# Optimization experiments

Hardware: AMD Instinct MI355X
Metric: run time of the kernel (lower is better)

Reference implementation:

```python
import jax, jax.numpy as jnp
import numpy as np

S = 2048   # seq_len
E = 1024   # embed_dim
N = 16     # num_heads
H = 64     # head_dim
CL = 1024  # context_length (sliding window)
BASE = 10000.0


def _rope(x, positions, base=BASE):
    # x: (seq, heads, head_dim); even/odd interleaved rotation per RotaryEmbedding
    hd = x.shape[-1]
    dim = hd // 2
    freqs = jnp.exp(-jnp.arange(dim, dtype=x.dtype) * (np.log(base) / dim))
    angles = positions.astype(x.dtype)[:, None] * freqs[None, :]  # (seq, dim)
    cos = jnp.cos(angles)[:, None, :]
    sin = jnp.sin(angles)[:, None, :]
    xe = x[..., ::2]
    xo = x[..., 1::2]
    re = xe * cos - xo * sin
    ro = xe * sin + xo * cos
    return jnp.zeros_like(x).at[..., ::2].set(re).at[..., 1::2].set(ro)


def setup_inputs() -> dict:
    key = jax.random.key(0)
    ks = jax.random.split(key, 9)
    scale = 1.0 / np.sqrt(E)  # keep logits O(1) like eqx.nn.Linear init
    x = jax.random.normal(ks[0], (S, E), jnp.float32)
    Wq = jax.random.normal(ks[1], (E, E), jnp.float32) * scale
    Wk = jax.random.normal(ks[2], (E, E), jnp.float32) * scale
    Wv = jax.random.normal(ks[3], (E, E), jnp.float32) * scale
    Wo = jax.random.normal(ks[4], (E, E), jnp.float32) * scale
    bq = jax.random.normal(ks[5], (E,), jnp.float32) * 0.01
    bk = jax.random.normal(ks[6], (E,), jnp.float32) * 0.01
    bv = jax.random.normal(ks[7], (E,), jnp.float32) * 0.01
    bo = jax.random.normal(ks[8], (E,), jnp.float32) * 0.01
    k_cache = jnp.zeros((CL - 1, N, H), jnp.float32)
    v_cache = jnp.zeros((CL - 1, N, H), jnp.float32)
    return {"x": x, "Wq": Wq, "bq": bq, "Wk": Wk, "bk": bk, "Wv": Wv,
            "bv": bv, "Wo": Wo, "bo": bo, "k_cache": k_cache,
            "v_cache": v_cache, "position": 0}


def reference(x, Wq, bq, Wk, bk, Wv, bv, Wo, bo, k_cache, v_cache, position):
    seq, emb = x.shape
    clm1, n, h = k_cache.shape  # context_length - 1
    cl = clm1 + 1
    # QKV projections (eqx.nn.Linear: W @ x + b, weight is (out, in))
    q = (x @ Wq.T + bq).reshape(seq, n, h)
    k = (x @ Wk.T + bk).reshape(seq, n, h)
    v = (x @ Wv.T + bv).reshape(seq, n, h)
    # RoPE offset by cache position
    pos = jnp.arange(seq) + position
    q = _rope(q, pos)
    k = _rope(k, pos)
    # Append to cache
    k = jnp.concatenate([k_cache, k], axis=0)  # (seq + cl - 1, n, h)
    v = jnp.concatenate([v_cache, v], axis=0)
    # Sliding-window + causal mask, exactly as SelfAttentionBlock.init_mask
    in_dim = seq + clm1
    m = jnp.tril(jnp.ones((in_dim, seq)))
    neg = 1.0 - jnp.tril(jnp.ones((in_dim, seq)), -cl)
    mask = (m * neg).astype(bool).T  # (seq_q, kv_len)
    # Masked SDPA (same math as jax.nn.dot_product_attention with bool mask)
    scores = jnp.einsum('qnh,knh->nqk', q, k) / jnp.sqrt(jnp.asarray(h, q.dtype))
    scores = jnp.where(mask[None], scores, jnp.asarray(-1e30, scores.dtype))
    attn = jax.nn.softmax(scores, axis=-1)
    o = jnp.einsum('nqk,knh->qnh', attn, v).reshape(seq, n * h)
    out = o @ Wo.T + bo
    new_k = k[-(cl - 1):]
    new_v = v[-(cl - 1):]
    return (out, new_k, new_v)
```

## Files before the change

kernel.cpp:

```cpp
#include <hip/hip_runtime.h>
#include <hip/hip_bf16.h>
#include <stdint.h>

#define SQ   2048
#define EMB  1024
#define NH   16
#define HD   64
#define CLM1 1023
#define KTOT 3071
#define KR   3136

typedef __attribute__((ext_vector_type(8))) short short8;
typedef __attribute__((ext_vector_type(4))) float f32x4;

__device__ __forceinline__ short bf16s(float f) {
  __hip_bfloat16 h = __float2bfloat16(f);
  return *reinterpret_cast<short*>(&h);
}

__device__ __forceinline__ float fexp2(float x) {
  float r;
  asm("v_exp_f32 %0, %1" : "=v"(r) : "v"(x));
  return r;
}

#define GLOAD16(g, l) __builtin_amdgcn_global_load_lds( \
    (const __attribute__((address_space(1))) void*)(g), \
    (__attribute__((address_space(3))) void*)(l), 16, 0, 0)

__global__ __launch_bounds__(256) void k_prep(const float* __restrict__ x,
                                              const float* __restrict__ Wq,
                                              const float* __restrict__ Wk,
                                              const float* __restrict__ Wv,
                                              const float* __restrict__ Wo,
                                              const float* __restrict__ bq,
                                              const float* __restrict__ bk,
                                              const float* __restrict__ bv,
                                              const float* __restrict__ kc,
                                              short* __restrict__ xb,
                                              short* __restrict__ wqkvb,
                                              short* __restrict__ wob,
                                              float* __restrict__ bqkv,
                                              short* __restrict__ Kc) {
  const int b = blockIdx.x;
  const int tid = threadIdx.x;
  if (b < 2048) {
    int i = b * 256 + tid;
    float4 v = ((const float4*)x)[i];
    short4 o; o.x = bf16s(v.x); o.y = bf16s(v.y); o.z = bf16s(v.z); o.w = bf16s(v.w);
    ((short4*)xb)[i] = o;
  } else if (b < 5120) {
    int i = (b - 2048) * 256 + tid;
    int seg = i >> 18;
    int loc = i & 262143;
    const float* W = (seg == 0) ? Wq : (seg == 1) ? Wk : Wv;
    float4 v = ((const float4*)W)[loc];
    short4 o; o.x = bf16s(v.x); o.y = bf16s(v.y); o.z = bf16s(v.z); o.w = bf16s(v.w);
    ((short4*)wqkvb)[i] = o;
  } else if (b < 6144) {
    int i = (b - 5120) * 256 + tid;
    float4 v = ((const float4*)Wo)[i];
    short4 o; o.x = bf16s(v.x); o.y = bf16s(v.y); o.z = bf16s(v.z); o.w = bf16s(v.w);
    ((short4*)wob)[i] = o;
  } else if (b < 10236) {
    int idx = (b - 6144) * 256 + tid;
    int h = idx & 63;
    int n = (idx >> 6) & 15;
    int i = idx >> 10;
    Kc[((size_t)n * KR + i) * HD + h] = bf16s(kc[idx]);
  } else {
    int i = (b - 10236) * 256 + tid;
    if (i < 3 * EMB) {
      float v = (i < EMB) ? bq[i] : (i < 2 * EMB) ? bk[i - EMB] : bv[i - 2 * EMB];
      bqkv[i] = v;
    }
  }
}

__global__ __launch_bounds__(256) void k_vt(const float* __restrict__ vc,
                                            const float* __restrict__ qkv,
                                            short* __restrict__ Vt,
                                            float* __restrict__ nv) {
  const int n = blockIdx.y;
  const int i0 = blockIdx.x * 64;
  const int tid = threadIdx.x;
  __shared__ short T[64][66];
  const int h = tid & 63;
  const int iq = tid >> 6;
#pragma unroll
  for (int e = 0; e < 16; ++e) {
    int il = iq + 4 * e;
    int i = i0 + il;
    float v;
    if (i < CLM1)      v = vc[((size_t)i * NH + n) * HD + h];
    else if (i < KTOT) v = qkv[(size_t)(i - CLM1) * (3 * EMB) + 2 * EMB + n * HD + h];
    else               v = 0.0f;
    T[il][h] = bf16s(v);
    if (i >= 2048 && i < KTOT)
      nv[((size_t)(i - 2048) * NH + n) * HD + h] = v;
  }
  __syncthreads();
  const int h2 = tid >> 2;
  const int c0 = (tid & 3) * 16;
  short* dst = &Vt[((size_t)n * HD + h2) * KR + i0 + c0];
#pragma unroll
  for (int c = 0; c < 2; ++c) {
    short8 o;
#pragma unroll
    for (int e = 0; e < 8; ++e) o[e] = T[c0 + c * 8 + e][h2];
    *(short8*)&dst[c * 8] = o;
  }
}

__global__ __launch_bounds__(256) void k_gemm(const short* __restrict__ A,
                                              const short* __restrict__ B,
                                              const float* __restrict__ bias,
                                              float* __restrict__ C,
                                              int M, int N, int K) {
  __shared__ short As[4][128 * 32];
  __shared__ short Bs[4][128 * 32];
  const int tid = threadIdx.x;
  const int lane = tid & 63;
  const int wid = tid >> 6;
  const int wr = wid >> 1, wc = wid & 1;
  const int row0 = blockIdx.x * 128, col0 = blockIdx.y * 128;
  const int lr = lane & 15;
  const int lk = (lane >> 4) * 8;
  const int sr = tid >> 2;
  const int sc = (tid & 3) * 8;
  const short* Ag = A + (size_t)(row0 + sr) * K + sc;
  const short* Bg = B + (size_t)(col0 + sr) * K + sc;

  f32x4 acc[4][4] = {};

#define GSTAGE(k0_, b_) { \
    GLOAD16(Ag + (k0_),                  &As[b_][tid * 8]); \
    GLOAD16(Ag + (size_t)64 * K + (k0_), &As[b_][2048 + tid * 8]); \
    GLOAD16(Bg + (k0_),                  &Bs[b_][tid * 8]); \
    GLOAD16(Bg + (size_t)64 * K + (k0_), &Bs[b_][2048 + tid * 8]); }

  const int nk = K >> 5;
  GSTAGE(0, 0);
  GSTAGE(32, 1);
  for (int ki = 0; ki < nk; ++ki) {
    int kp = (ki + 2 < nk) ? ki + 2 : nk - 1;
    GSTAGE(kp * 32, (ki + 2) & 3);
    asm volatile("s_waitcnt vmcnt(8)" ::: "memory");
    __builtin_amdgcn_s_barrier();
    const short* Ab = As[ki & 3];
    const short* Bb = Bs[ki & 3];
    short8 a[4], bfr[4];
#pragma unroll
    for (int m = 0; m < 4; ++m)
      a[m] = *(const short8*)&Ab[(wr * 64 + m * 16 + lr) * 32 + lk];
#pragma unroll
    for (int nn = 0; nn < 4; ++nn)
      bfr[nn] = *(const short8*)&Bb[(wc * 64 + nn * 16 + lr) * 32 + lk];
#pragma unroll
    for (int m = 0; m < 4; ++m)
#pragma unroll
      for (int nn = 0; nn < 4; ++nn)
        acc[m][nn] = __builtin_amdgcn_mfma_f32_16x16x32_bf16(a[m], bfr[nn], acc[m][nn], 0, 0, 0);
  }
#undef GSTAGE

#pragma unroll
  for (int m = 0; m < 4; ++m) {
    int r = row0 + wr * 64 + m * 16 + (lane >> 4) * 4;
#pragma unroll
    for (int nn = 0; nn < 4; ++nn) {
      int c = col0 + wc * 64 + nn * 16 + lr;
      float bv = bias[c];
#pragma unroll
      for (int j = 0; j < 4; ++j)
        C[(size_t)(r + j) * N + c] = acc[m][nn][j] + bv;
    }
  }
}

__global__ __launch_bounds__(256) void k_gemmO(const short* __restrict__ A,
                                               const short* __restrict__ B,
                                               const float* __restrict__ bias,
                                               float* __restrict__ C,
                                               int M, int N, int K) {
  __shared__ short As[4][64 * 32];
  __shared__ short Bs[4][128 * 32];
  const int tid = threadIdx.x;
  const int lane = tid & 63;
  const int wid = tid >> 6;
  const int wr = wid >> 1, wc = wid & 1;
  const int row0 = blockIdx.x * 64, col0 = blockIdx.y * 128;
  const int lr = lane & 15;
  const int lk = (lane >> 4) * 8;
  const int sr = tid >> 2;
  const int sc = (tid & 3) * 8;
  const short* Ag = A + (size_t)(row0 + sr) * K + sc;
  const short* Bg = B + (size_t)(col0 + sr) * K + sc;

  f32x4 acc[2][4] = {};

#define GSTAGEO(k0_, b_) { \
    GLOAD16(Ag + (k0_),                  &As[b_][tid * 8]); \
    GLOAD16(Bg + (k0_),                  &Bs[b_][tid * 8]); \
    GLOAD16(Bg + (size_t)64 * K + (k0_), &Bs[b_][2048 + tid * 8]); }

  const int nk = K >> 5;
  GSTAGEO(0, 0);
  GSTAGEO(32, 1);
  for (int ki = 0; ki < nk; ++ki) {
    int kp = (ki + 2 < nk) ? ki + 2 : nk - 1;
    GSTAGEO(kp * 32, (ki + 2) & 3);
    asm volatile("s_waitcnt vmcnt(6)" ::: "memory");
    __builtin_amdgcn_s_barrier();
    const short* Ab = As[ki & 3];
    const short* Bb = Bs[ki & 3];
    short8 a[2], bfr[4];
#pragma unroll
    for (int m = 0; m < 2; ++m)
      a[m] = *(const short8*)&Ab[(wr * 32 + m * 16 + lr) * 32 + lk];
#pragma unroll
    for (int nn = 0; nn < 4; ++nn)
      bfr[nn] = *(const short8*)&Bb[(wc * 64 + nn * 16 + lr) * 32 + lk];
#pragma unroll
    for (int m = 0; m < 2; ++m)
#pragma unroll
      for (int nn = 0; nn < 4; ++nn)
        acc[m][nn] = __builtin_amdgcn_mfma_f32_16x16x32_bf16(a[m], bfr[nn], acc[m][nn], 0, 0, 0);
  }
#undef GSTAGEO

#pragma unroll
  for (int m = 0; m < 2; ++m) {
    int r = row0 + wr * 32 + m * 16 + (lane >> 4) * 4;
#pragma unroll
    for (int nn = 0; nn < 4; ++nn) {
      int c = col0 + wc * 64 + nn * 16 + lr;
      float bv = bias[c];
#pragma unroll
      for (int j = 0; j < 4; ++j)
        C[(size_t)(r + j) * N + c] = acc[m][nn][j] + bv;
    }
  }
}

__global__ __launch_bounds__(256) void k_rope(const float* __restrict__ qkv,
                                              const int* __restrict__ pos,
                                              short* __restrict__ qb,
                                              short* __restrict__ Kc,
                                              float* __restrict__ nk) {
  int j = blockIdx.x;
  int tid = threadIdx.x;
  __shared__ float cs[32], sn[32];
  if (tid < 32) {
    float fr = expf(-(float)tid * 0.28782313662425575f);
    float ang = (float)(j + pos[0]) * fr;
    cs[tid] = cosf(ang);
    sn[tid] = sinf(ang);
  }
  __syncthreads();
  const float* base = qkv + (size_t)j * (3 * EMB);
#pragma unroll
  for (int p = tid; p < NH * 32; p += 256) {
    int n = p >> 5, d = p & 31;
    float c = cs[d], s = sn[d];
    float qe = base[n * HD + 2 * d], qo = base[n * HD + 2 * d + 1];
    float qre = qe * c - qo * s;
    float qro = qe * s + qo * c;
    size_t qoff = ((size_t)n * SQ + j) * HD + 2 * d;
    qb[qoff] = bf16s(qre);
    qb[qoff + 1] = bf16s(qro);
    float ke = base[EMB + n * HD + 2 * d], ko = base[EMB + n * HD + 2 * d + 1];
    float kre = ke * c - ko * s;
    float kro = ke * s + ko * c;
    int i = CLM1 + j;
    size_t koff = ((size_t)n * KR + i) * HD + 2 * d;
    Kc[koff] = bf16s(kre);
    Kc[koff + 1] = bf16s(kro);
    if (j >= 1025) {
      size_t noff = (((size_t)(j - 1025)) * NH + n) * HD + 2 * d;
      nk[noff] = kre;
      nk[noff + 1] = kro;
    }
  }
}

__global__ __launch_bounds__(256) void k_attn(const short* __restrict__ qb,
                                              const short* __restrict__ Kc,
                                              const short* __restrict__ Vt,
                                              short* __restrict__ ob) {
  const int bid = blockIdx.x;
  const int hi = bid >> 8;
  const int rr = bid & 255;
  const int n = ((rr & 7) << 1) | hi;
  const int q0 = (rr >> 3) * 64;
  const int tid = threadIdx.x;
  const int wid = tid >> 6;
  const int lane = tid & 63;
  const int lr = lane & 15;
  const int lq = lane >> 4;
  const int lk = lq * 8;
  const int qw = q0 + wid * 16;

  __shared__ short Ks[4][32 * 64];
  __shared__ short Vs[4][64 * 32];
  __shared__ short Pl[4][16][40];

  const short* Qh = qb + (size_t)n * SQ * HD;
  const short* Kh = Kc + (size_t)n * KR * HD;
  const short* Vh = Vt + (size_t)n * HD * KR;

  const int skey = tid >> 3;
  const int ksrc = ((tid & 7) ^ (skey & 7)) << 3;
  const int vh = tid >> 2;
  const int vsrc = ((tid & 3) ^ ((vh >> 1) & 3)) << 3;

  short8 qf0 = *(const short8*)&Qh[(qw + lr) * HD + lk];
  short8 qf1 = *(const short8*)&Qh[(qw + lr) * HD + 32 + lk];

  f32x4 o0 = {0,0,0,0}, o1 = {0,0,0,0}, o2 = {0,0,0,0}, o3 = {0,0,0,0};
  f32x4 ps = {0,0,0,0};
  const float C1 = 0.125f * 1.44269504f;
  const float C2 = -14.0f * 1.44269504f;

  const int kslotA = ((lq ^ (lr & 7)) << 3);
  const int kslotB = (((4 ^ lq) ^ (lr & 7)) << 3);
  const int vslot = ((lq ^ ((lr >> 1) & 3)) << 3);

#define ASTAGE(tt, b_) { int kt_ = q0 + (tt) * 32; \
    GLOAD16(&Kh[(size_t)(kt_ + skey) * HD + ksrc], &Ks[b_][tid * 8]); \
    GLOAD16(&Vh[(size_t)vh * KR + kt_ + vsrc],     &Vs[b_][tid * 8]); }

  ASTAGE(0, 0);
  ASTAGE(1, 1);
  for (int t = 0; t < 34; ++t) {
    int tp = (t + 2 < 34) ? t + 2 : 33;
    ASTAGE(tp, (t + 2) & 3);
    asm volatile("s_waitcnt vmcnt(4)" ::: "memory");
    __builtin_amdgcn_s_barrier();
    const int kt = q0 + t * 32;
    const bool active = (kt + 31 >= qw) && (kt <= qw + 1038);
    if (active) {
      const short* K0 = Ks[t & 3];
      short8 kf0 = *(const short8*)&K0[lr * 64 + kslotA];
      short8 kf1 = *(const short8*)&K0[lr * 64 + kslotB];
      short8 kf2 = *(const short8*)&K0[(16 + lr) * 64 + kslotA];
      short8 kf3 = *(const short8*)&K0[(16 + lr) * 64 + kslotB];
      f32x4 s0 = {0,0,0,0}, s1 = {0,0,0,0};
      s0 = __builtin_amdgcn_mfma_f32_16x16x32_bf16(qf0, kf0, s0, 0, 0, 0);
      s0 = __builtin_amdgcn_mfma_f32_16x16x32_bf16(qf1, kf1, s0, 0, 0, 0);
      s1 = __builtin_amdgcn_mfma_f32_16x16x32_bf16(qf0, kf2, s1, 0, 0, 0);
      s1 = __builtin_amdgcn_mfma_f32_16x16x32_bf16(qf1, kf3, s1, 0, 0, 0);

      float p0[4], p1[4];
      const bool interior = (kt >= qw + 15) && (kt + 31 <= qw + 1023);
      if (interior) {
#pragma unroll
        for (int r = 0; r < 4; ++r) {
          p0[r] = fexp2(fmaf(s0[r], C1, C2));
          p1[r] = fexp2(fmaf(s1[r], C1, C2));
        }
      } else {
        const int key0 = kt + lr, key1 = kt + 16 + lr;
#pragma unroll
        for (int r = 0; r < 4; ++r) {
          int qj = qw + lq * 4 + r;
          float v0 = (key0 >= qj && key0 <= qj + 1023) ? s0[r] : -1e30f;
          float v1 = (key1 >= qj && key1 <= qj + 1023) ? s1[r] : -1e30f;
          p0[r] = fexp2(fmaf(v0, C1, C2));
          p1[r] = fexp2(fmaf(v1, C1, C2));
        }
      }
#pragma unroll
      for (int r = 0; r < 4; ++r) {
        ps[r] += p0[r] + p1[r];
        int prow = lq * 4 + r;
        Pl[wid][prow][lr] = bf16s(p0[r]);
        Pl[wid][prow][lr + 16] = bf16s(p1[r]);
      }
      asm volatile("s_waitcnt lgkmcnt(0)" ::: "memory");
      short8 pf = *(const short8*)&Pl[wid][lr][lk];
      const short* V0 = Vs[t & 3];
      o0 = __builtin_amdgcn_mfma_f32_16x16x32_bf16(pf, *(const short8*)&V0[(0 * 16 + lr) * 32 + vslot], o0, 0, 0, 0);
      o1 = __builtin_amdgcn_mfma_f32_16x16x32_bf16(pf, *(const short8*)&V0[(1 * 16 + lr) * 32 + vslot], o1, 0, 0, 0);
      o2 = __builtin_amdgcn_mfma_f32_16x16x32_bf16(pf, *(const short8*)&V0[(2 * 16 + lr) * 32 + vslot], o2, 0, 0, 0);
      o3 = __builtin_amdgcn_mfma_f32_16x16x32_bf16(pf, *(const short8*)&V0[(3 * 16 + lr) * 32 + vslot], o3, 0, 0, 0);
    }
  }
#undef ASTAGE

#pragma unroll
  for (int r = 0; r < 4; ++r) {
    float rs = ps[r];
    rs += __shfl_xor(rs, 1);
    rs += __shfl_xor(rs, 2);
    rs += __shfl_xor(rs, 4);
    rs += __shfl_xor(rs, 8);
    float inv = 1.0f / rs;
    int qj = qw + lq * 4 + r;
    size_t rowoff = (size_t)qj * EMB + n * HD;
    ob[rowoff + 0 * 16 + lr] = bf16s(o0[r] * inv);
    ob[rowoff + 1 * 16 + lr] = bf16s(o1[r] * inv);
    ob[rowoff + 2 * 16 + lr] = bf16s(o2[r] * inv);
    ob[rowoff + 3 * 16 + lr] = bf16s(o3[r] * inv);
  }
}

extern "C" void kernel_launch(void* const* d_in, const int* in_sizes, int n_in,
                              void* d_out, int out_size, void* d_ws, size_t ws_size,
                              hipStream_t stream) {
  const float* x      = (const float*)d_in[0];
  const float* Wq     = (const float*)d_in[1];
  const float* bq     = (const float*)d_in[2];
  const float* Wk     = (const float*)d_in[3];
  const float* bk     = (const float*)d_in[4];
  const float* Wv     = (const float*)d_in[5];
  const float* bv     = (const float*)d_in[6];
  const float* Wo     = (const float*)d_in[7];
  const float* bo     = (const float*)d_in[8];
  const float* kcache = (const float*)d_in[9];
  const float* vcache = (const float*)d_in[10];
  const int*   pos    = (const int*)d_in[11];

  float* out = (float*)d_out;
  float* nk  = out + (size_t)SQ * EMB;
  float* nv  = nk + (size_t)CLM1 * NH * HD;

  char* w = (char*)d_ws;
  size_t o0 = 0;
  short* xb    = (short*)(w + o0); o0 += (size_t)SQ * EMB * 2;
  short* wqkvb = (short*)(w + o0); o0 += (size_t)3 * EMB * EMB * 2;
  short* wob   = (short*)(w + o0); o0 += (size_t)EMB * EMB * 2;
  float* bqkv  = (float*)(w + o0); o0 += (size_t)3 * EMB * 4;
  float* qkv   = (float*)(w + o0); o0 += (size_t)SQ * 3 * EMB * 4;
  short* qbuf  = (short*)(w + o0); o0 += (size_t)NH * SQ * HD * 2;
  short* Kc    = (short*)(w + o0); o0 += (size_t)NH * KR * HD * 2;
  short* Vt    = (short*)(w + o0); o0 += (size_t)NH * HD * KR * 2;
  short* ob    = (short*)(w + o0); o0 += (size_t)SQ * EMB * 2;

  k_prep<<<10248, 256, 0, stream>>>(x, Wq, Wk, Wv, Wo, bq, bk, bv, kcache,
                                    xb, wqkvb, wob, bqkv, Kc);
  k_gemm<<<dim3(SQ / 128, 3 * EMB / 128), 256, 0, stream>>>(xb, wqkvb, bqkv, qkv, SQ, 3 * EMB, EMB);
  k_rope<<<SQ, 256, 0, stream>>>(qkv, pos, qbuf, Kc, nk);
  k_vt<<<dim3(48, NH), 256, 0, stream>>>(vcache, qkv, Vt, nv);
  k_attn<<<512, 256, 0, stream>>>(qbuf, Kc, Vt, ob);
  k_gemmO<<<dim3(SQ / 64, EMB / 128), 256, 0, stream>>>(ob, wob, bo, out, SQ, EMB, EMB);
}
```

Baseline: 183.5 us.

## Fuse RoPE and V/cache writes into QKV GEMM epilogue with precomputed trig tables

```diff
diff --git a/kernel.cpp b/kernel.cpp
--- a/kernel.cpp
+++ b/kernel.cpp
@@ -37,11 +37,14 @@
                                               const float* __restrict__ bk,
                                               const float* __restrict__ bv,
                                               const float* __restrict__ kc,
+                                              const int* __restrict__ pos,
                                               short* __restrict__ xb,
                                               short* __restrict__ wqkvb,
                                               short* __restrict__ wob,
                                               float* __restrict__ bqkv,
-                                              short* __restrict__ Kc) {
+                                              short* __restrict__ Kc,
+                                              float* __restrict__ tabc,
+                                              float* __restrict__ tabs) {
   const int b = blockIdx.x;
   const int tid = threadIdx.x;
   if (b < 2048) {
@@ -68,19 +71,140 @@
     int n = (idx >> 6) & 15;
     int i = idx >> 10;
     Kc[((size_t)n * KR + i) * HD + h] = bf16s(kc[idx]);
-  } else {
+  } else if (b < 10248) {
     int i = (b - 10236) * 256 + tid;
     if (i < 3 * EMB) {
       float v = (i < EMB) ? bq[i] : (i < 2 * EMB) ? bk[i - EMB] : bv[i - 2 * EMB];
       bqkv[i] = v;
     }
+  } else {
+    int idx = (b - 10248) * 256 + tid;
+    int d = idx >> 11;
+    int j = idx & 2047;
+    float fr = expf(-(float)d * 0.28782313662425575f);
+    float ang = (float)(j + pos[0]) * fr;
+    float s, c;
+    sincosf(ang, &s, &c);
+    tabc[d * SQ + j] = c;
+    tabs[d * SQ + j] = s;
+  }
+}
+
+__global__ __launch_bounds__(256) void k_gemmQKV(const short* __restrict__ A,
+                                                 const short* __restrict__ B,
+                                                 const float* __restrict__ bias,
+                                                 const float* __restrict__ tabc,
+                                                 const float* __restrict__ tabs,
+                                                 short* __restrict__ qbuf,
+                                                 short* __restrict__ Kc,
+                                                 short* __restrict__ vrows,
+                                                 float* __restrict__ nk,
+                                                 float* __restrict__ nv) {
+  __shared__ short As[4][128 * 32];
+  __shared__ short Bs[4][128 * 32];
+  const int K = EMB;
+  const int tid = threadIdx.x;
+  const int lane = tid & 63;
+  const int wid = tid >> 6;
+  const int wr = wid >> 1, wc = wid & 1;
+  const int row0 = blockIdx.x * 128, col0 = blockIdx.y * 128;
+  const int lr = lane & 15;
+  const int lq = lane >> 4;
+  const int lk = lq * 8;
+  const int sr = tid >> 2;
+  const int sc = (tid & 3) * 8;
+  const short* Ag = A + (size_t)(row0 + sr) * K + sc;
+  const short* Bg = B + (size_t)(col0 + sr) * K + sc;
+
+  f32x4 acc[4][4] = {};
+
+#define GSTAGE(k0_, b_) { \
+    GLOAD16(Ag + (k0_),                  &As[b_][tid * 8]); \
+    GLOAD16(Ag + (size_t)64 * K + (k0_), &As[b_][2048 + tid * 8]); \
+    GLOAD16(Bg + (k0_),                  &Bs[b_][tid * 8]); \
+    GLOAD16(Bg + (size_t)64 * K + (k0_), &Bs[b_][2048 + tid * 8]); }
+
+  const int nkk = K >> 5;
+  GSTAGE(0, 0);
+  GSTAGE(32, 1);
+  for (int ki = 0; ki < nkk; ++ki) {
+    int kp = (ki + 2 < nkk) ? ki + 2 : nkk - 1;
+    GSTAGE(kp * 32, (ki + 2) & 3);
+    asm volatile("s_waitcnt vmcnt(8)" ::: "memory");
+    __builtin_amdgcn_s_barrier();
+    const short* Ab = As[ki & 3];
+    const short* Bb = Bs[ki & 3];
+    short8 a[4], bfr[4];
+#pragma unroll
+    for (int m = 0; m < 4; ++m)
+      a[m] = *(const short8*)&Ab[(wr * 64 + m * 16 + lr) * 32 + lk];
+#pragma unroll
+    for (int nn = 0; nn < 4; ++nn)
+      bfr[nn] = *(const short8*)&Bb[(wc * 64 + nn * 16 + lr) * 32 + lk];
+#pragma unroll
+    for (int m = 0; m < 4; ++m)
+#pragma unroll
+      for (int nn = 0; nn < 4; ++nn)
+        acc[m][nn] = __builtin_amdgcn_mfma_f32_16x16x32_bf16(a[m], bfr[nn], acc[m][nn], 0, 0, 0);
+  }
+#undef GSTAGE
+
+  const int cseg = col0 >> 10;
+#pragma unroll
+  for (int m = 0; m < 4; ++m) {
+    const int rbase = row0 + wr * 64 + m * 16 + lq * 4;
+#pragma unroll
+    for (int nn = 0; nn < 4; ++nn) {
+      const int cl = wc * 64 + nn * 16 + lr;
+      const int c = col0 + cl;
+      const float bv = bias[c];
+      float v[4];
+#pragma unroll
+      for (int j = 0; j < 4; ++j) v[j] = acc[m][nn][j] + bv;
+      if (cseg < 2) {
+        const int d = (cl >> 1) & 31;
+        const float4 cs4 = *(const float4*)&tabc[d * SQ + rbase];
+        const float4 sn4 = *(const float4*)&tabs[d * SQ + rbase];
+        const float cs[4] = {cs4.x, cs4.y, cs4.z, cs4.w};
+        const float sn[4] = {sn4.x, sn4.y, sn4.z, sn4.w};
+        const bool odd = (c & 1);
+        float out[4];
+#pragma unroll
+        for (int j = 0; j < 4; ++j) {
+          float part = __shfl_xor(v[j], 1);
+          out[j] = odd ? fmaf(part, sn[j], v[j] * cs[j])
+                       : fmaf(part, -sn[j], v[j] * cs[j]);
+        }
+        const int n = (c >> 6) & 15;
+        const int h = c & 63;
+        if (cseg == 0) {
+#pragma unroll
+          for (int j = 0; j < 4; ++j)
+            qbuf[((size_t)n * SQ + rbase + j) * HD + h] = bf16s(out[j]);
+        } else {
+#pragma unroll
+          for (int j = 0; j < 4; ++j) {
+            Kc[((size_t)n * KR + CLM1 + rbase + j) * HD + h] = bf16s(out[j]);
+            if (rbase + j >= 1025)
+              nk[((size_t)(rbase + j - 1025) * NH + n) * HD + h] = out[j];
+          }
+        }
+      } else {
+        const int cv = c - 2048;
+#pragma unroll
+        for (int j = 0; j < 4; ++j) {
+          vrows[(size_t)(rbase + j) * EMB + cv] = bf16s(v[j]);
+          if (rbase + j >= 1025)
+            nv[(size_t)(rbase + j - 1025) * EMB + cv] = v[j];
+        }
+      }
+    }
   }
 }
 
 __global__ __launch_bounds__(256) void k_vt(const float* __restrict__ vc,
-                                            const float* __restrict__ qkv,
-                                            short* __restrict__ Vt,
-                                            float* __restrict__ nv) {
+                                            const short* __restrict__ vrows,
+                                            short* __restrict__ Vt) {
   const int n = blockIdx.y;
   const int i0 = blockIdx.x * 64;
   const int tid = threadIdx.x;
@@ -91,13 +215,11 @@
   for (int e = 0; e < 16; ++e) {
     int il = iq + 4 * e;
     int i = i0 + il;
-    float v;
-    if (i < CLM1)      v = vc[((size_t)i * NH + n) * HD + h];
-    else if (i < KTOT) v = qkv[(size_t)(i - CLM1) * (3 * EMB) + 2 * EMB + n * HD + h];
-    else               v = 0.0f;
-    T[il][h] = bf16s(v);
-    if (i >= 2048 && i < KTOT)
-      nv[((size_t)(i - 2048) * NH + n) * HD + h] = v;
+    short s;
+    if (i < CLM1)      s = bf16s(vc[((size_t)i * NH + n) * HD + h]);
+    else if (i < KTOT) s = vrows[(size_t)(i - CLM1) * EMB + n * HD + h];
+    else               s = 0;
+    T[il][h] = s;
   }
   __syncthreads();
   const int h2 = tid >> 2;
@@ -109,72 +231,6 @@
 #pragma unroll
     for (int e = 0; e < 8; ++e) o[e] = T[c0 + c * 8 + e][h2];
     *(short8*)&dst[c * 8] = o;
-  }
-}
-
-__global__ __launch_bounds__(256) void k_gemm(const short* __restrict__ A,
-                                              const short* __restrict__ B,
-                                              const float* __restrict__ bias,
-                                              float* __restrict__ C,
-                                              int M, int N, int K) {
-  __shared__ short As[4][128 * 32];
-  __shared__ short Bs[4][128 * 32];
-  const int tid = threadIdx.x;
-  const int lane = tid & 63;
-  const int wid = tid >> 6;
-  const int wr = wid >> 1, wc = wid & 1;
-  const int row0 = blockIdx.x * 128, col0 = blockIdx.y * 128;
-  const int lr = lane & 15;
-  const int lk = (lane >> 4) * 8;
-  const int sr = tid >> 2;
-  const int sc = (tid & 3) * 8;
-  const short* Ag = A + (size_t)(row0 + sr) * K + sc;
-  const short* Bg = B + (size_t)(col0 + sr) * K + sc;
-
-  f32x4 acc[4][4] = {};
-
-#define GSTAGE(k0_, b_) { \
-    GLOAD16(Ag + (k0_),                  &As[b_][tid * 8]); \
-    GLOAD16(Ag + (size_t)64 * K + (k0_), &As[b_][2048 + tid * 8]); \
-    GLOAD16(Bg + (k0_),                  &Bs[b_][tid * 8]); \
-    GLOAD16(Bg + (size_t)64 * K + (k0_), &Bs[b_][2048 + tid * 8]); }
-
-  const int nk = K >> 5;
-  GSTAGE(0, 0);
-  GSTAGE(32, 1);
-  for (int ki = 0; ki < nk; ++ki) {
-    int kp = (ki + 2 < nk) ? ki + 2 : nk - 1;
-    GSTAGE(kp * 32, (ki + 2) & 3);
-    asm volatile("s_waitcnt vmcnt(8)" ::: "memory");
-    __builtin_amdgcn_s_barrier();
-    const short* Ab = As[ki & 3];
-    const short* Bb = Bs[ki & 3];
-    short8 a[4], bfr[4];
-#pragma unroll
-    for (int m = 0; m < 4; ++m)
-      a[m] = *(const short8*)&Ab[(wr * 64 + m * 16 + lr) * 32 + lk];
-#pragma unroll
-    for (int nn = 0; nn < 4; ++nn)
-      bfr[nn] = *(const short8*)&Bb[(wc * 64 + nn * 16 + lr) * 32 + lk];
-#pragma unroll
-    for (int m = 0; m < 4; ++m)
-#pragma unroll
-      for (int nn = 0; nn < 4; ++nn)
-        acc[m][nn] = __builtin_amdgcn_mfma_f32_16x16x32_bf16(a[m], bfr[nn], acc[m][nn], 0, 0, 0);
-  }
-#undef GSTAGE
-
-#pragma unroll
-  for (int m = 0; m < 4; ++m) {
-    int r = row0 + wr * 64 + m * 16 + (lane >> 4) * 4;
-#pragma unroll
-    for (int nn = 0; nn < 4; ++nn) {
-      int c = col0 + wc * 64 + nn * 16 + lr;
-      float bv = bias[c];
-#pragma unroll
-      for (int j = 0; j < 4; ++j)
-        C[(size_t)(r + j) * N + c] = acc[m][nn][j] + bv;
-    }
   }
 }
 
@@ -239,47 +295,6 @@
 #pragma unroll
       for (int j = 0; j < 4; ++j)
         C[(size_t)(r + j) * N + c] = acc[m][nn][j] + bv;
-    }
-  }
-}
-
-__global__ __launch_bounds__(256) void k_rope(const float* __restrict__ qkv,
-                                              const int* __restrict__ pos,
-                                              short* __restrict__ qb,
-                                              short* __restrict__ Kc,
-                                              float* __restrict__ nk) {
-  int j = blockIdx.x;
-  int tid = threadIdx.x;
-  __shared__ float cs[32], sn[32];
-  if (tid < 32) {
-    float fr = expf(-(float)tid * 0.28782313662425575f);
-    float ang = (float)(j + pos[0]) * fr;
-    cs[tid] = cosf(ang);
-    sn[tid] = sinf(ang);
-  }
-  __syncthreads();
-  const float* base = qkv + (size_t)j * (3 * EMB);
-#pragma unroll
-  for (int p = tid; p < NH * 32; p += 256) {
-    int n = p >> 5, d = p & 31;
-    float c = cs[d], s = sn[d];
-    float qe = base[n * HD + 2 * d], qo = base[n * HD + 2 * d + 1];
-    float qre = qe * c - qo * s;
-    float qro = qe * s + qo * c;
-    size_t qoff = ((size_t)n * SQ + j) * HD + 2 * d;
-    qb[qoff] = bf16s(qre);
-    qb[qoff + 1] = bf16s(qro);
-    float ke = base[EMB + n * HD + 2 * d], ko = base[EMB + n * HD + 2 * d + 1];
-    float kre = ke * c - ko * s;
-    float kro = ke * s + ko * c;
-    int i = CLM1 + j;
-    size_t koff = ((size_t)n * KR + i) * HD + 2 * d;
-    Kc[koff] = bf16s(kre);
-    Kc[koff + 1] = bf16s(kro);
-    if (j >= 1025) {
-      size_t noff = (((size_t)(j - 1025)) * NH + n) * HD + 2 * d;
-      nk[noff] = kre;
-      nk[noff + 1] = kro;
     }
   }
 }
@@ -431,17 +446,19 @@
   short* wqkvb = (short*)(w + o0); o0 += (size_t)3 * EMB * EMB * 2;
   short* wob   = (short*)(w + o0); o0 += (size_t)EMB * EMB * 2;
   float* bqkv  = (float*)(w + o0); o0 += (size_t)3 * EMB * 4;
-  float* qkv   = (float*)(w + o0); o0 += (size_t)SQ * 3 * EMB * 4;
+  float* tabc  = (float*)(w + o0); o0 += (size_t)32 * SQ * 4;
+  float* tabs  = (float*)(w + o0); o0 += (size_t)32 * SQ * 4;
   short* qbuf  = (short*)(w + o0); o0 += (size_t)NH * SQ * HD * 2;
   short* Kc    = (short*)(w + o0); o0 += (size_t)NH * KR * HD * 2;
+  short* vrows = (short*)(w + o0); o0 += (size_t)SQ * EMB * 2;
   short* Vt    = (short*)(w + o0); o0 += (size_t)NH * HD * KR * 2;
   short* ob    = (short*)(w + o0); o0 += (size_t)SQ * EMB * 2;
 
-  k_prep<<<10248, 256, 0, stream>>>(x, Wq, Wk, Wv, Wo, bq, bk, bv, kcache,
-                                    xb, wqkvb, wob, bqkv, Kc);
-  k_gemm<<<dim3(SQ / 128, 3 * EMB / 128), 256, 0, stream>>>(xb, wqkvb, bqkv, qkv, SQ, 3 * EMB, EMB);
-  k_rope<<<SQ, 256, 0, stream>>>(qkv, pos, qbuf, Kc, nk);
-  k_vt<<<dim3(48, NH), 256, 0, stream>>>(vcache, qkv, Vt, nv);
+  k_prep<<<10504, 256, 0, stream>>>(x, Wq, Wk, Wv, Wo, bq, bk, bv, kcache, pos,
+                                    xb, wqkvb, wob, bqkv, Kc, tabc, tabs);
+  k_gemmQKV<<<dim3(SQ / 128, 3 * EMB / 128), 256, 0, stream>>>(
+      xb, wqkvb, bqkv, tabc, tabs, qbuf, Kc, vrows, nk, nv);
+  k_vt<<<dim3(48, NH), 256, 0, stream>>>(vcache, vrows, Vt);
   k_attn<<<512, 256, 0, stream>>>(qbuf, Kc, Vt, ob);
   k_gemmO<<<dim3(SQ / 64, EMB / 128), 256, 0, stream>>>(ob, wob, bo, out, SQ, EMB, EMB);
 }
```

Measured after the change: 177.6 us. 3.2% less time.
